# Optimization experiments

Hardware: AMD Instinct MI355X
Metric: run time of the kernel (lower is better)

## Reference

```python
import jax, jax.numpy as jnp
import numpy as np

HC = 4            # hc_mult
HIDDEN = 4096
SINKHORN_ITERS = 5
HC_EPS = 1e-5
NORM_EPS = 1e-6
B, S = 2, 4096


def setup_inputs() -> dict:
    key = jax.random.key(0)
    k0, k1, k2, k3 = jax.random.split(key, 4)
    mix = (2 + HC) * HC  # 24
    return {
        "hidden_streams": jax.random.normal(k0, (B, S, HC, HIDDEN), dtype=jnp.float32),
        # small init so sigmoid/softmax gates stay in a sane range
        "fn": jax.random.normal(k1, (mix, HC * HIDDEN), dtype=jnp.float32) * 0.01,
        "base": jax.random.normal(k2, (mix,), dtype=jnp.float32),
        "scale": jax.random.normal(k3, (3,), dtype=jnp.float32),
    }


def reference(hidden_streams, fn, base, scale):
    hc = HC
    # flatten streams: [B, S, hc*hidden]
    flat = hidden_streams.reshape(hidden_streams.shape[0], hidden_streams.shape[1], -1).astype(jnp.float32)
    rsqrt = jax.lax.rsqrt(jnp.mean(jnp.square(flat), axis=-1, keepdims=True) + NORM_EPS)
    # packed projection to mix=(2+hc)*hc gate logits, RMS-scaled
    mix = jnp.einsum("bsd,md->bsm", flat, fn.astype(jnp.float32)) * rsqrt
    pre_scale, post_scale, comb_scale = scale[0], scale[1], scale[2]
    pre = jax.nn.sigmoid(mix[..., :hc] * pre_scale + base[:hc]) + HC_EPS
    post = 2.0 * jax.nn.sigmoid(mix[..., hc:2 * hc] * post_scale + base[hc:2 * hc])
    comb_logit = mix[..., 2 * hc:].reshape(*mix.shape[:-1], hc, hc) * comb_scale + base[2 * hc:].reshape(hc, hc)
    comb = jax.nn.softmax(comb_logit, axis=-1) + HC_EPS
    comb = comb / (jnp.sum(comb, axis=-2, keepdims=True) + HC_EPS)
    for _ in range(SINKHORN_ITERS - 1):
        comb = comb / (jnp.sum(comb, axis=-1, keepdims=True) + HC_EPS)
        comb = comb / (jnp.sum(comb, axis=-2, keepdims=True) + HC_EPS)
    return pre, post, comb
```

## Files before the change

### kernel.cpp

```cpp
#include <hip/hip_runtime.h>
#include <hip/hip_bf16.h>
#include <math.h>
#include <stdint.h>

#define HC 4
#define DIM 16384
#define MIXN 24
#define NROWS 8192
#define KSPLIT 32
#define KSL 512
#define NSTEPS 16
#define NSTREAM 8
#define ROWS_PER_STREAM 1024
#define NTILES 64
#define NBUF 3
#define THREADS1 512
#define HC_EPS 1e-5f
#define NORM_EPS 1e-6f

#define PRE_OFF 0
#define POST_OFF (NROWS * HC)
#define COMB_OFF (2 * NROWS * HC)

typedef float f32x4 __attribute__((ext_vector_type(4)));
typedef float accf4 __attribute__((ext_vector_type(4)));
typedef short bf16x8 __attribute__((ext_vector_type(8)));
typedef short bf16x4 __attribute__((ext_vector_type(4)));

__device__ __forceinline__ short f2bf(float x) {
    union { __hip_bfloat16 h; short s; } u;
    u.h = __float2bfloat16(x);
    return u.s;
}

__global__ __launch_bounds__(THREADS1) void hyper_k1(
    const float* __restrict__ hs,
    const float* __restrict__ fn,
    float* __restrict__ ws)
{
    const int tid  = threadIdx.x;
    const int wave = tid >> 6;
    const int lane = tid & 63;
    const int l15  = lane & 15;
    const int kg   = lane >> 4;
    const int ks     = blockIdx.x & (KSPLIT - 1);
    const int stream = blockIdx.x >> 5;

    __shared__ __align__(16) short s_fn[2][NSTEPS][512];
    __shared__ __align__(16) short s_a[NBUF][NSTEPS][512];
    __shared__ float sC[8][400];

    #pragma unroll 1
    for (int p = 0; p < 4; ++p) {
        const int idx  = p * THREADS1 + tid;
        const int kgf  = idx & 3;
        const int s    = (idx >> 2) & 15;
        const int c    = (idx >> 6) & 15;
        const int tile = idx >> 10;
        const int col  = tile ? (c + 8) : c;
        const float* g = fn + (size_t)col * DIM + ks * KSL + s * 32 + kgf * 8;
        const f32x4 v0 = *(const f32x4*)g;
        const f32x4 v1 = *(const f32x4*)(g + 4);
        bf16x8 b = { f2bf(v0.x), f2bf(v0.y), f2bf(v0.z), f2bf(v0.w),
                     f2bf(v1.x), f2bf(v1.y), f2bf(v1.z), f2bf(v1.w) };
        *(bf16x8*)&s_fn[tile][s][(kgf * 16 + c) * 8] = b;
    }
    __syncthreads();

    const int st_slo = lane >> 3;
    const int st_kg  = (lane >> 1) & 3;
    const int st_e   = (lane & 1) * 4;
    const int sr0 = 2 * wave, sr1 = 2 * wave + 1;

    f32x4 RA0, RA1, RA2, RA3;
    f32x4 RB0, RB1, RB2, RB3;

#define ISSUE(P0, P1, P2, P3, T) do { \
    const float* g0 = hs + (size_t)(stream * ROWS_PER_STREAM + (T) * 16 + sr0) * DIM + ks * KSL; \
    const float* g1 = hs + (size_t)(stream * ROWS_PER_STREAM + (T) * 16 + sr1) * DIM + ks * KSL; \
    P0 = *(const f32x4*)(g0 +   0 + lane * 4); \
    P1 = *(const f32x4*)(g0 + 256 + lane * 4); \
    P2 = *(const f32x4*)(g1 +   0 + lane * 4); \
    P3 = *(const f32x4*)(g1 + 256 + lane * 4); \
} while (0)

#define WR1(BUF, Rj, r, j) do { \
    const int s_ = (j) * 8 + st_slo; \
    int byte_ = ((s_ * 64 + st_kg * 16 + (r)) * 16) + st_e * 2; \
    byte_ ^= ((s_ & 7) << 4); \
    bf16x4 v_ = { f2bf(Rj.x), f2bf(Rj.y), f2bf(Rj.z), f2bf(Rj.w) }; \
    *(bf16x4*)((char*)(&s_a[BUF][0][0]) + byte_) = v_; \
} while (0)

#define WRALL(BUF, P0, P1, P2, P3) do { \
    WR1(BUF, P0, sr0, 0); WR1(BUF, P1, sr0, 1); \
    WR1(BUF, P2, sr1, 0); WR1(BUF, P3, sr1, 1); \
} while (0)

    ISSUE(RA0, RA1, RA2, RA3, 0);
    ISSUE(RB0, RB1, RB2, RB3, 1);
    WRALL(0, RA0, RA1, RA2, RA3);
    ISSUE(RA0, RA1, RA2, RA3, 2);

    int buf = 0;
    #pragma unroll 2
    for (int t = 0; t < NTILES; ++t) {
        asm volatile("s_waitcnt lgkmcnt(0)" ::: "memory");
        __builtin_amdgcn_s_barrier();
        __builtin_amdgcn_sched_barrier(0);

        accf4 acc0 = {0.f, 0.f, 0.f, 0.f};
        accf4 acc1 = {0.f, 0.f, 0.f, 0.f};
        accf4 accS = {0.f, 0.f, 0.f, 0.f};
        #pragma unroll
        for (int i = 0; i < 2; ++i) {
            const int s = wave * 2 + i;
            int ab = ((s * 64 + lane) * 16) ^ ((s & 7) << 4);
            const bf16x8 af = *(const bf16x8*)((const char*)(&s_a[buf][0][0]) + ab);
            const bf16x8 b0 = *(const bf16x8*)&s_fn[0][s][lane * 8];
            const bf16x8 b1 = *(const bf16x8*)&s_fn[1][s][lane * 8];
            acc0 = __builtin_amdgcn_mfma_f32_16x16x32_bf16(af, b0, acc0, 0, 0, 0);
            acc1 = __builtin_amdgcn_mfma_f32_16x16x32_bf16(af, b1, acc1, 0, 0, 0);
            accS = __builtin_amdgcn_mfma_f32_16x16x32_bf16(af, af, accS, 0, 0, 0);
        }

        #pragma unroll
        for (int i = 0; i < 4; ++i)
            sC[wave][(kg * 4 + i) * 25 + l15] = acc0[i];
        if (l15 >= 8) {
            #pragma unroll
            for (int i = 0; i < 4; ++i)
                sC[wave][(kg * 4 + i) * 25 + l15 + 8] = acc1[i];
        }
        #pragma unroll
        for (int i = 0; i < 4; ++i)
            if (l15 == kg * 4 + i) sC[wave][l15 * 25 + 24] = accS[i];

        asm volatile("s_waitcnt lgkmcnt(0)" ::: "memory");
        __builtin_amdgcn_s_barrier();
        __builtin_amdgcn_sched_barrier(0);

        if (tid < 400) {
            const float v = sC[0][tid] + sC[1][tid] + sC[2][tid] + sC[3][tid]
                          + sC[4][tid] + sC[5][tid] + sC[6][tid] + sC[7][tid];
            ws[((size_t)(stream * NTILES + t) * KSPLIT + ks) * 400 + tid] = v;
        }

        if (t + 1 < NTILES) {
            const int nbuf = (buf + 1 == NBUF) ? 0 : buf + 1;
            if ((t & 1) == 0) {
                WRALL(nbuf, RB0, RB1, RB2, RB3);
                if (t + 3 < NTILES) ISSUE(RB0, RB1, RB2, RB3, t + 3);
            } else {
                WRALL(nbuf, RA0, RA1, RA2, RA3);
                if (t + 3 < NTILES) ISSUE(RA0, RA1, RA2, RA3, t + 3);
            }
        }
        buf = (buf + 1 == NBUF) ? 0 : buf + 1;
    }
#undef ISSUE
#undef WR1
#undef WRALL
}

__global__ __launch_bounds__(256) void hyper_k2(
    const float* __restrict__ ws,
    const float* __restrict__ base,
    const float* __restrict__ scale,
    float* __restrict__ out)
{
    const int r  = blockIdx.x * 256 + threadIdx.x;
    const int rt = r >> 4, rr = r & 15;

    float v[25];
    #pragma unroll
    for (int c = 0; c < 25; ++c) v[c] = 0.f;
    #pragma unroll 1
    for (int ks = 0; ks < KSPLIT; ++ks) {
        const float* w = ws + ((size_t)rt * KSPLIT + ks) * 400 + rr * 25;
        #pragma unroll
        for (int c = 0; c < 25; ++c) v[c] += w[c];
    }

    const float rs = 1.0f / sqrtf(v[24] * (1.0f / (float)DIM) + NORM_EPS);
    const float s0 = scale[0], s1 = scale[1], s2 = scale[2];

    #pragma unroll
    for (int i = 0; i < HC; ++i) {
        const float z = v[i] * rs * s0 + base[i];
        out[PRE_OFF + r * HC + i] = 1.0f / (1.0f + expf(-z)) + HC_EPS;
    }
    #pragma unroll
    for (int i = 0; i < HC; ++i) {
        const float z = v[HC + i] * rs * s1 + base[HC + i];
        out[POST_OFF + r * HC + i] = 2.0f / (1.0f + expf(-z));
    }

    float c[HC][HC];
    #pragma unroll
    for (int i = 0; i < HC; ++i) {
        float l[HC];
        #pragma unroll
        for (int j = 0; j < HC; ++j)
            l[j] = v[2 * HC + i * HC + j] * rs * s2 + base[2 * HC + i * HC + j];
        const float mx = fmaxf(fmaxf(l[0], l[1]), fmaxf(l[2], l[3]));
        float e[HC];
        float sum = 0.0f;
        #pragma unroll
        for (int j = 0; j < HC; ++j) { e[j] = expf(l[j] - mx); sum += e[j]; }
        const float inv = 1.0f / sum;
        #pragma unroll
        for (int j = 0; j < HC; ++j) c[i][j] = e[j] * inv + HC_EPS;
    }
    #pragma unroll
    for (int j = 0; j < HC; ++j) {
        const float cs = c[0][j] + c[1][j] + c[2][j] + c[3][j] + HC_EPS;
        const float inv = 1.0f / cs;
        c[0][j] *= inv; c[1][j] *= inv; c[2][j] *= inv; c[3][j] *= inv;
    }
    #pragma unroll
    for (int it = 0; it < 4; ++it) {
        #pragma unroll
        for (int i = 0; i < HC; ++i) {
            const float rsum = c[i][0] + c[i][1] + c[i][2] + c[i][3] + HC_EPS;
            const float inv = 1.0f / rsum;
            c[i][0] *= inv; c[i][1] *= inv; c[i][2] *= inv; c[i][3] *= inv;
        }
        #pragma unroll
        for (int j = 0; j < HC; ++j) {
            const float cs = c[0][j] + c[1][j] + c[2][j] + c[3][j] + HC_EPS;
            const float inv = 1.0f / cs;
            c[0][j] *= inv; c[1][j] *= inv; c[2][j] *= inv; c[3][j] *= inv;
        }
    }
    #pragma unroll
    for (int i = 0; i < HC; ++i)
        #pragma unroll
        for (int j = 0; j < HC; ++j)
            out[COMB_OFF + r * (HC * HC) + i * HC + j] = c[i][j];
}

extern "C" void kernel_launch(void* const* d_in, const int* in_sizes, int n_in,
                              void* d_out, int out_size, void* d_ws, size_t ws_size,
                              hipStream_t stream) {
    const float* hs    = (const float*)d_in[0];
    const float* fn    = (const float*)d_in[1];
    const float* base  = (const float*)d_in[2];
    const float* scale = (const float*)d_in[3];
    float* out = (float*)d_out;
    float* ws  = (float*)d_ws;

    hyper_k1<<<KSPLIT * NSTREAM, THREADS1, 0, stream>>>(hs, fn, ws);
    hyper_k2<<<NROWS / 256, 256, 0, stream>>>(ws, base, scale, out);
}
```

Baseline: 133.5 us.

## Double the projection grid and parallelize the split-K reduction with wave shuffles

The projection kernel now uses 16 row streams of 512 rows each instead of 8 of 1024, doubling the block count. To compensate, it drops to two LDS staging buffers. Partial sums are written as per-row, per-K-slice records of 32 floats. The epilogue kernel assigns 32 lanes per row, one lane per K slice, and reduces them with xor shuffles. This replaces the old scheme of one thread serially summing 32 strided records. The goal is better CU occupancy and latency hiding in the main kernel and much more parallel reduction loads in the epilogue, at the cost of a slightly larger workspace and idle lanes in the gate math.

```diff
diff --git a/kernel.cpp b/kernel.cpp
--- a/kernel.cpp
+++ b/kernel.cpp
@@ -10,11 +10,12 @@
 #define KSPLIT 32
 #define KSL 512
 #define NSTEPS 16
-#define NSTREAM 8
-#define ROWS_PER_STREAM 1024
-#define NTILES 64
-#define NBUF 3
+#define NSTREAM 16
+#define ROWS_PER_STREAM 512
+#define NTILES 32
+#define NBUF 2
 #define THREADS1 512
+#define WREC 32
 #define HC_EPS 1e-5f
 #define NORM_EPS 1e-6f
 
@@ -141,13 +142,15 @@
         __builtin_amdgcn_sched_barrier(0);
 
         if (tid < 400) {
+            const int rr = tid / 25, c = tid % 25;
             const float v = sC[0][tid] + sC[1][tid] + sC[2][tid] + sC[3][tid]
                           + sC[4][tid] + sC[5][tid] + sC[6][tid] + sC[7][tid];
-            ws[((size_t)(stream * NTILES + t) * KSPLIT + ks) * 400 + tid] = v;
+            const int row = stream * ROWS_PER_STREAM + t * 16 + rr;
+            ws[((size_t)row * KSPLIT + ks) * WREC + c] = v;
         }
 
         if (t + 1 < NTILES) {
-            const int nbuf = (buf + 1 == NBUF) ? 0 : buf + 1;
+            const int nbuf = buf ^ 1;
             if ((t & 1) == 0) {
                 WRALL(nbuf, RB0, RB1, RB2, RB3);
                 if (t + 3 < NTILES) ISSUE(RB0, RB1, RB2, RB3, t + 3);
@@ -156,7 +159,7 @@
                 if (t + 3 < NTILES) ISSUE(RA0, RA1, RA2, RA3, t + 3);
             }
         }
-        buf = (buf + 1 == NBUF) ? 0 : buf + 1;
+        buf ^= 1;
     }
 #undef ISSUE
 #undef WR1
@@ -169,18 +172,21 @@
     const float* __restrict__ scale,
     float* __restrict__ out)
 {
-    const int r  = blockIdx.x * 256 + threadIdx.x;
-    const int rt = r >> 4, rr = r & 15;
+    const int tid = threadIdx.x;
+    const int row = blockIdx.x * 8 + (tid >> 5);
+    const int ks  = tid & 31;
 
     float v[25];
-    #pragma unroll
-    for (int c = 0; c < 25; ++c) v[c] = 0.f;
-    #pragma unroll 1
-    for (int ks = 0; ks < KSPLIT; ++ks) {
-        const float* w = ws + ((size_t)rt * KSPLIT + ks) * 400 + rr * 25;
-        #pragma unroll
-        for (int c = 0; c < 25; ++c) v[c] += w[c];
-    }
+    const float* w = ws + ((size_t)row * KSPLIT + ks) * WREC;
+    #pragma unroll
+    for (int c = 0; c < 25; ++c) v[c] = w[c];
+
+    #pragma unroll
+    for (int off = 16; off >= 1; off >>= 1)
+        #pragma unroll
+        for (int c = 0; c < 25; ++c) v[c] += __shfl_xor(v[c], off, 32);
+
+    if (ks != 0) return;
 
     const float rs = 1.0f / sqrtf(v[24] * (1.0f / (float)DIM) + NORM_EPS);
     const float s0 = scale[0], s1 = scale[1], s2 = scale[2];
@@ -188,12 +194,12 @@
     #pragma unroll
     for (int i = 0; i < HC; ++i) {
         const float z = v[i] * rs * s0 + base[i];
-        out[PRE_OFF + r * HC + i] = 1.0f / (1.0f + expf(-z)) + HC_EPS;
+        out[PRE_OFF + row * HC + i] = 1.0f / (1.0f + expf(-z)) + HC_EPS;
     }
     #pragma unroll
     for (int i = 0; i < HC; ++i) {
         const float z = v[HC + i] * rs * s1 + base[HC + i];
-        out[POST_OFF + r * HC + i] = 2.0f / (1.0f + expf(-z));
+        out[POST_OFF + row * HC + i] = 2.0f / (1.0f + expf(-z));
     }
 
     float c[HC][HC];
@@ -237,7 +243,7 @@
     for (int i = 0; i < HC; ++i)
         #pragma unroll
         for (int j = 0; j < HC; ++j)
-            out[COMB_OFF + r * (HC * HC) + i * HC + j] = c[i][j];
+            out[COMB_OFF + row * (HC * HC) + i * HC + j] = c[i][j];
 }
 
 extern "C" void kernel_launch(void* const* d_in, const int* in_sizes, int n_in,
@@ -251,5 +257,5 @@
     float* ws  = (float*)d_ws;
 
     hyper_k1<<<KSPLIT * NSTREAM, THREADS1, 0, stream>>>(hs, fn, ws);
-    hyper_k2<<<NROWS / 256, 256, 0, stream>>>(ws, base, scale, out);
-}
+    hyper_k2<<<NROWS / 8, 256, 0, stream>>>(ws, base, scale, out);
+}
```

Measured after the change: 133.6 us. About the same (+0.1%).
